# Performance work log

Measured on AMD Instinct MI355X. Metric: run time of the kernel, lower is better.

The kernel has to match this reference:

```python
import jax, jax.numpy as jnp
import numpy as np
import math

B, T, D_MODEL, N_HEADS = 4, 2048, 1024, 16
D_HEAD = D_MODEL // N_HEADS


def _rope_freqs(t, d_head):
    inv = 1.0 / (10000.0 ** (np.arange(0, d_head, 2, dtype=np.float32) / d_head))
    ang = np.arange(t, dtype=np.float32)[:, None] * inv[None, :]  # (T, d_head//2)
    return jnp.asarray(np.cos(ang)), jnp.asarray(np.sin(ang))


def setup_inputs() -> dict:
    key = jax.random.key(0)
    k1, k2, k3, k4, k5 = jax.random.split(key, 5)
    s = 1.0 / math.sqrt(D_MODEL)
    x = jax.random.normal(k1, (B, T, D_MODEL), dtype=jnp.float32)
    mask = jnp.triu(jnp.ones((T, T), dtype=bool), k=1)  # causal: mask future positions
    freqs_cos, freqs_sin = _rope_freqs(T, D_HEAD)
    qkv_w = jax.random.uniform(k2, (3 * D_MODEL, D_MODEL), jnp.float32, -s, s)
    qkv_b = jax.random.uniform(k3, (3 * D_MODEL,), jnp.float32, -s, s)
    proj_w = jax.random.uniform(k4, (D_MODEL, D_MODEL), jnp.float32, -s, s)
    proj_b = jax.random.uniform(k5, (D_MODEL,), jnp.float32, -s, s)
    return {"x": x, "mask": mask, "freqs_cos": freqs_cos, "freqs_sin": freqs_sin,
            "qkv_w": qkv_w, "qkv_b": qkv_b, "proj_w": proj_w, "proj_b": proj_b}


def _apply_rope(t, cos, sin):
    # t: (B, H, T, D_HEAD); cos/sin: (T, D_HEAD//2), broadcast over B, H
    tp = t.reshape(*t.shape[:-1], -1, 2)
    a, b = tp[..., 0], tp[..., 1]
    out_r = a * cos - b * sin
    out_i = a * sin + b * cos
    return jnp.stack([out_r, out_i], axis=-1).reshape(t.shape)


def reference(x, mask, freqs_cos, freqs_sin, qkv_w, qkv_b, proj_w, proj_b):
    Bx, Tx, C = x.shape
    qkv = x @ qkv_w.T + qkv_b  # (B, T, 3C)
    q, k, v = jnp.split(qkv, 3, axis=-1)
    def heads(z):
        return z.reshape(Bx, Tx, N_HEADS, D_HEAD).transpose(0, 2, 1, 3)  # (B,H,T,dh)
    q, k, v = heads(q), heads(k), heads(v)
    q = _apply_rope(q, freqs_cos, freqs_sin)
    k = _apply_rope(k, freqs_cos, freqs_sin)
    att = jnp.einsum('bhqd,bhkd->bhqk', q, k) / math.sqrt(D_HEAD)
    att = jnp.where(mask, -jnp.inf, att)
    att = jax.nn.softmax(att, axis=-1)
    out = jnp.einsum('bhqk,bhkd->bhqd', att, v)
    out = out.transpose(0, 2, 1, 3).reshape(Bx, Tx, C)
    return out @ proj_w.T + proj_b
```

## Files before the change

### kernel.cpp

```cpp
#include <hip/hip_runtime.h>
#include <stdint.h>

#define BB 4
#define TT 2048
#define CC 1024
#define HH 16
#define DH 64
#define NQKV 3072

typedef __bf16 bf16_t;
typedef __attribute__((ext_vector_type(8))) __bf16 bf16x8;
typedef __attribute__((ext_vector_type(4))) float f32x4;

#define MFMA16(a, b, c) __builtin_amdgcn_mfma_f32_16x16x32_bf16((a), (b), (c), 0, 0, 0)

__device__ __forceinline__ void gll16(const void* g, void* l) {
  typedef const __attribute__((address_space(1))) void* gp_t;
  typedef __attribute__((address_space(3))) void* lp_t;
  __builtin_amdgcn_global_load_lds((gp_t)(uintptr_t)g, (lp_t)(uintptr_t)l, 16, 0, 0);
}

__global__ __launch_bounds__(256) void cvt_k(const float* __restrict__ src,
                                             bf16_t* __restrict__ dst, int n) {
  const int i8 = (blockIdx.x * 256 + threadIdx.x) * 8;
  if (i8 < n) {
    const f32x4 a = *(const f32x4*)(src + i8);
    const f32x4 b = *(const f32x4*)(src + i8 + 4);
    bf16x8 r;
    r[0] = (bf16_t)a[0]; r[1] = (bf16_t)a[1]; r[2] = (bf16_t)a[2]; r[3] = (bf16_t)a[3];
    r[4] = (bf16_t)b[0]; r[5] = (bf16_t)b[1]; r[6] = (bf16_t)b[2]; r[7] = (bf16_t)b[3];
    *(bf16x8*)(dst + i8) = r;
  }
}

template <int EPI>
__global__ __launch_bounds__(256) void gemm_k(
    const bf16_t* __restrict__ A, const bf16_t* __restrict__ W,
    const float* __restrict__ bias,
    const float* __restrict__ fcos, const float* __restrict__ fsin,
    void* __restrict__ out0v, bf16_t* __restrict__ out1,
    bf16_t* __restrict__ out2) {
  __shared__ bf16_t Alds[2][128 * 32];
  __shared__ bf16_t Blds[2][128 * 32];
  const int K = 1024;
  const int tid = threadIdx.x;
  const int lane = tid & 63, wave = tid >> 6;
  const int quad = lane >> 4, c = lane & 15;
  const int wm = wave >> 1, wn = wave & 1;
  const int mbase = blockIdx.y * 128, nbase = blockIdx.x * 128;

  f32x4 acc[4][4];
#pragma unroll
  for (int i = 0; i < 4; ++i)
#pragma unroll
    for (int j = 0; j < 4; ++j) acc[i][j] = (f32x4){0.f, 0.f, 0.f, 0.f};

  const int ch0 = tid, ch1 = tid + 256;
  const bf16_t* ag0 = A + (mbase + (ch0 >> 2)) * K + (ch0 & 3) * 8;
  const bf16_t* ag1 = A + (mbase + (ch1 >> 2)) * K + (ch1 & 3) * 8;
  const bf16_t* bg0 = W + (nbase + (ch0 >> 2)) * K + (ch0 & 3) * 8;
  const bf16_t* bg1 = W + (nbase + (ch1 >> 2)) * K + (ch1 & 3) * 8;

  for (int k0 = 0; k0 < K; k0 += 64) {
    __syncthreads();
    gll16(ag0 + k0, &Alds[0][ch0 * 8]);
    gll16(ag1 + k0, &Alds[0][ch1 * 8]);
    gll16(bg0 + k0, &Blds[0][ch0 * 8]);
    gll16(bg1 + k0, &Blds[0][ch1 * 8]);
    gll16(ag0 + k0 + 32, &Alds[1][ch0 * 8]);
    gll16(ag1 + k0 + 32, &Alds[1][ch1 * 8]);
    gll16(bg0 + k0 + 32, &Blds[1][ch0 * 8]);
    gll16(bg1 + k0 + 32, &Blds[1][ch1 * 8]);
    __syncthreads();
#pragma unroll
    for (int half = 0; half < 2; ++half) {
      bf16x8 af[4], bfr[4];
#pragma unroll
      for (int mi = 0; mi < 4; ++mi)
        af[mi] = *(const bf16x8*)&Alds[half][(wm * 64 + mi * 16 + c) * 32 + quad * 8];
#pragma unroll
      for (int ni = 0; ni < 4; ++ni)
        bfr[ni] = *(const bf16x8*)&Blds[half][(wn * 64 + ni * 16 + c) * 32 + quad * 8];
#pragma unroll
      for (int mi = 0; mi < 4; ++mi)
#pragma unroll
        for (int ni = 0; ni < 4; ++ni)
          acc[mi][ni] = MFMA16(af[mi], bfr[ni], acc[mi][ni]);
    }
  }

  const float qscale = 0.18033688011112042f;
#pragma unroll
  for (int mi = 0; mi < 4; ++mi) {
#pragma unroll
    for (int ni = 0; ni < 4; ++ni) {
      const int n = nbase + wn * 64 + ni * 16 + c;
      const float bv = bias[n];
#pragma unroll
      for (int r = 0; r < 4; ++r) {
        const int m = mbase + wm * 64 + mi * 16 + quad * 4 + r;
        float v = acc[mi][ni][r] + bv;
        if (EPI == 0) {
          bf16_t* out0 = (bf16_t*)out0v;
          const int sel = n >> 10;
          const int nl = n & 1023;
          const int h = nl >> 6, d = nl & 63;
          const int b = m >> 11, t = m & 2047;
          const int dst = ((b * HH + h) * TT + t) * DH + d;
          if (sel < 2) {
            const float pv = __shfl_xor(v, 1, 64);
            const int d2 = d >> 1;
            const float cs = fcos[t * 32 + d2];
            const float sn = fsin[t * 32 + d2];
            float o = ((d & 1) == 0) ? (v * cs - pv * sn) : (pv * sn + v * cs);
            if (sel == 0) {
              o *= qscale;
              out0[dst] = (bf16_t)o;
            } else {
              out1[dst] = (bf16_t)o;
            }
          } else {
            out2[dst] = (bf16_t)v;
          }
        } else {
          float* outf = (float*)out0v;
          outf[m * CC + n] = v;
        }
      }
    }
  }
}

__global__ __launch_bounds__(256, 4) void attn_k(const bf16_t* __restrict__ Q,
                                                 const bf16_t* __restrict__ Kv,
                                                 const bf16_t* __restrict__ V,
                                                 bf16_t* __restrict__ O) {
  __shared__ bf16_t KS[2][64 * 64];
  __shared__ bf16_t VtS[2][64 * 64];
  __shared__ bf16_t PS[4][16 * 64];

  const int tid = threadIdx.x;
  const int lane = tid & 63, wave = tid >> 6;
  const int quad = lane >> 4, c = lane & 15;
  const int bi = blockIdx.x;
  const int pair = bi & 15, h = (bi >> 4) & 15, b = bi >> 8;
  const int qtA = pair, qtB = 31 - pair;
  const int nA = qtA + 1;

  const bf16_t* Qh = Q + ((b * HH + h) * TT) * DH;
  const bf16_t* Kh = Kv + ((b * HH + h) * TT) * DH;
  const bf16_t* Vh = V + ((b * HH + h) * TT) * DH;

  const f32x4 zero4 = {0.f, 0.f, 0.f, 0.f};
  bf16x8 ones8;
#pragma unroll
  for (int i = 0; i < 8; ++i) ones8[i] = (bf16_t)1.0f;

  const int krow0 = tid >> 3, kc8 = tid & 7, krow1 = krow0 + 32;
  const bf16_t* kbase0 = Kh + krow0 * DH + kc8 * 8;
  const bf16_t* kbase1 = Kh + krow1 * DH + kc8 * 8;
  const int vsb = tid >> 2, vjp = tid & 3;
  const int vrg = vsb & 7, vc8 = vsb >> 3;
  const int vd0 = vc8 * 8 + vjp * 2, vd1 = vd0 + 1;
  const bf16_t* vbase = Vh + vrg * 8 * DH + vd0;

  const int sw = c & 7;
  const int e0 = c * 64 + (quad ^ sw) * 8;
  const int e1 = c * 64 + ((quad + 4) ^ sw) * 8;

  bf16x8 kr0, kr1;
  uint32_t vr[8];
  auto load_tile = [&](int eoff) {
    kr0 = *(const bf16x8*)(kbase0 + eoff);
    kr1 = *(const bf16x8*)(kbase1 + eoff);
    const bf16_t* vp = vbase + eoff;
#pragma unroll
    for (int i = 0; i < 8; ++i) vr[i] = *(const uint32_t*)(vp + i * DH);
  };
  auto store_tile = [&](int buf) {
    *(bf16x8*)&KS[buf][(krow0 * 8 + (kc8 ^ (krow0 & 7))) * 8] = kr0;
    *(bf16x8*)&KS[buf][(krow1 * 8 + (kc8 ^ (krow1 & 7))) * 8] = kr1;
    union { bf16x8 v; uint16_t u[8]; } colA, colB;
#pragma unroll
    for (int i = 0; i < 8; ++i) {
      colA.u[i] = (uint16_t)(vr[i] & 0xffffu);
      colB.u[i] = (uint16_t)(vr[i] >> 16);
    }
    *(bf16x8*)&VtS[buf][(vd0 * 8 + (vrg ^ (vd0 & 7))) * 8] = colA.v;
    *(bf16x8*)&VtS[buf][(vd1 * 8 + (vrg ^ (vd1 & 7))) * 8] = colB.v;
  };

  int qtbase = qtA * 64;
  bf16x8 qf0 = *(const bf16x8*)(Qh + (qtbase + wave * 16 + c) * DH + quad * 8);
  bf16x8 qf1 = *(const bf16x8*)(Qh + (qtbase + wave * 16 + c) * DH + 32 + quad * 8);

  f32x4 o_acc[4] = {zero4, zero4, zero4, zero4};
  float m_r[4] = {-1e30f, -1e30f, -1e30f, -1e30f};
  float l_r[4] = {0.f, 0.f, 0.f, 0.f};

  auto write_O = [&](int qtb) {
#pragma unroll
    for (int r = 0; r < 4; ++r) {
      const int qg = qtb + wave * 16 + quad * 4 + r;
      const float inv = 1.0f / l_r[r];
#pragma unroll
      for (int ni = 0; ni < 4; ++ni)
        O[(b * TT + qg) * CC + h * 64 + ni * 16 + c] =
            (bf16_t)(o_acc[ni][r] * inv);
    }
  };

  load_tile(0);
  store_tile(0);
  __syncthreads();
  int coff = 0;
  int kkey = 0;

#define ATTN_ITER(FI, CUR)                                                     \
  {                                                                            \
    const int fi_ = (FI);                                                      \
    const bool pre_ = fi_ < 32;                                                \
    const int noff_ = (fi_ + 1 == nA) ? 0 : coff + 64 * DH;                    \
    if (pre_) load_tile(noff_);                                                \
    bf16x8 kf0[4], kf1[4];                                                     \
    _Pragma("unroll") for (int ni = 0; ni < 4; ++ni) {                         \
      kf0[ni] = *(const bf16x8*)&KS[CUR][ni * 1024 + e0];                      \
      kf1[ni] = *(const bf16x8*)&KS[CUR][ni * 1024 + e1];                      \
    }                                                                          \
    f32x4 s[4];                                                                \
    _Pragma("unroll") for (int ni = 0; ni < 4; ++ni) {                         \
      f32x4 t = MFMA16(qf0, kf0[ni], zero4);                                   \
      t = MFMA16(qf1, kf1[ni], t);                                             \
      s[ni] = t;                                                               \
    }                                                                          \
    const int minq_ = qtbase + wave * 16;                                      \
    if (kkey + 63 > minq_) {                                                   \
      _Pragma("unroll") for (int ni = 0; ni < 4; ++ni)                         \
          _Pragma("unroll") for (int r = 0; r < 4; ++r) {                      \
        const int key_ = kkey + ni * 16 + c;                                   \
        const int qg_ = minq_ + quad * 4 + r;                                  \
        if (key_ > qg_) s[ni][r] = -1e30f;                                     \
      }                                                                        \
    }                                                                          \
    float alpha[4];                                                            \
    _Pragma("unroll") for (int r = 0; r < 4; ++r) {                            \
      float mx = fmaxf(fmaxf(s[0][r], s[1][r]), fmaxf(s[2][r], s[3][r]));      \
      mx = fmaxf(mx, __shfl_xor(mx, 1, 64));                                   \
      mx = fmaxf(mx, __shfl_xor(mx, 2, 64));                                   \
      mx = fmaxf(mx, __shfl_xor(mx, 4, 64));                                   \
      mx = fmaxf(mx, __shfl_xor(mx, 8, 64));                                   \
      const float mnew = fmaxf(m_r[r], mx);                                    \
      alpha[r] = __builtin_amdgcn_exp2f(m_r[r] - mnew);                        \
      m_r[r] = mnew;                                                           \
    }                                                                          \
    _Pragma("unroll") for (int ni = 0; ni < 4; ++ni)                           \
        _Pragma("unroll") for (int r = 0; r < 4; ++r) {                        \
      const float p = __builtin_amdgcn_exp2f(s[ni][r] - m_r[r]);               \
      const int prow_ = quad * 4 + r, pcol_ = ni * 16 + c;                     \
      PS[wave][(prow_ * 8 + ((pcol_ >> 3) ^ (prow_ & 7))) * 8 + (pcol_ & 7)] = \
          (bf16_t)p;                                                           \
    }                                                                          \
    _Pragma("unroll") for (int r = 0; r < 4; ++r) {                            \
      _Pragma("unroll") for (int ni = 0; ni < 4; ++ni)                         \
          o_acc[ni][r] *= alpha[r];                                            \
    }                                                                          \
    asm volatile("s_waitcnt lgkmcnt(0)" ::: "memory");                         \
    const bf16x8 p0 = *(const bf16x8*)&PS[wave][e0];                           \
    const bf16x8 p1 = *(const bf16x8*)&PS[wave][e1];                           \
    f32x4 rs = MFMA16(p0, ones8, zero4);                                       \
    rs = MFMA16(p1, ones8, rs);                                                \
    _Pragma("unroll") for (int ni = 0; ni < 4; ++ni) {                         \
      const bf16x8 v0 = *(const bf16x8*)&VtS[CUR][ni * 1024 + e0];             \
      const bf16x8 v1 = *(const bf16x8*)&VtS[CUR][ni * 1024 + e1];             \
      o_acc[ni] = MFMA16(p0, v0, o_acc[ni]);                                   \
      o_acc[ni] = MFMA16(p1, v1, o_acc[ni]);                                   \
    }                                                                          \
    _Pragma("unroll") for (int r = 0; r < 4; ++r)                              \
        l_r[r] = l_r[r] * alpha[r] + rs[r];                                    \
    if (fi_ == nA - 1) {                                                       \
      write_O(qtbase);                                                         \
      qtbase = qtB * 64;                                                       \
      qf0 = *(const bf16x8*)(Qh + (qtbase + wave * 16 + c) * DH + quad * 8);   \
      qf1 = *(const bf16x8*)(Qh + (qtbase + wave * 16 + c) * DH + 32 +         \
                             quad * 8);                                        \
      _Pragma("unroll") for (int r = 0; r < 4; ++r) {                          \
        m_r[r] = -1e30f;                                                       \
        l_r[r] = 0.f;                                                          \
      }                                                                        \
      _Pragma("unroll") for (int ni = 0; ni < 4; ++ni) o_acc[ni] = zero4;      \
    }                                                                          \
    if (pre_) store_tile(1 - (CUR));                                           \
    __syncthreads();                                                           \
    coff = noff_;                                                              \
    kkey = (fi_ + 1 == nA) ? 0 : kkey + 64;                                    \
  }

  for (int fj = 0; fj < 16; ++fj) {
    ATTN_ITER(2 * fj, 0)
    ATTN_ITER(2 * fj + 1, 1)
  }
  ATTN_ITER(32, 0)
#undef ATTN_ITER

  write_O(qtbase);
}

extern "C" void kernel_launch(void* const* d_in, const int* in_sizes, int n_in,
                              void* d_out, int out_size, void* d_ws,
                              size_t ws_size, hipStream_t stream) {
  const float *x = nullptr, *fcos = nullptr, *fsin = nullptr;
  const float *qkv_w = nullptr, *qkv_b = nullptr, *proj_w = nullptr, *proj_b = nullptr;
  for (int i = 0; i < n_in; ++i) {
    const int s = in_sizes[i];
    const float* p = (const float*)d_in[i];
    if (s == BB * TT * CC) x = p;
    else if (s == TT * (DH / 2)) { if (!fcos) fcos = p; else fsin = p; }
    else if (s == NQKV * CC) qkv_w = p;
    else if (s == NQKV) qkv_b = p;
    else if (s == CC * CC) proj_w = p;
    else if (s == CC) proj_b = p;
  }

  const size_t NE = (size_t)BB * TT * CC;
  bf16_t* Qb = (bf16_t*)d_ws;
  bf16_t* Kb = Qb + NE;
  bf16_t* Vb = Kb + NE;
  bf16_t* Ob = Vb + NE;
  bf16_t* xb = Ob;
  bf16_t* wqkvb = (bf16_t*)d_out;
  bf16_t* wpb = Qb;

  cvt_k<<<dim3((int)(NE / 2048)), 256, 0, stream>>>(x, xb, (int)NE);
  cvt_k<<<dim3(NQKV * CC / 2048), 256, 0, stream>>>(qkv_w, wqkvb, NQKV * CC);

  gemm_k<0><<<dim3(NQKV / 128, (BB * TT) / 128), 256, 0, stream>>>(
      xb, wqkvb, qkv_b, fcos, fsin, (void*)Qb, Kb, Vb);
  attn_k<<<dim3(BB * HH * 16), 256, 0, stream>>>(Qb, Kb, Vb, Ob);
  cvt_k<<<dim3(CC * CC / 2048), 256, 0, stream>>>(proj_w, wpb, CC * CC);
  gemm_k<1><<<dim3(CC / 128, (BB * TT) / 128), 256, 0, stream>>>(
      Ob, wpb, proj_b, nullptr, nullptr, d_out, nullptr, nullptr);
}
```

Before: 329.5 us.

## Swizzle GEMM LDS tiles and read attention K fragments directly from global

Measured after the change: 397.7 us. 1.21x slower.

```diff
diff --git a/kernel.cpp b/kernel.cpp
--- a/kernel.cpp
+++ b/kernel.cpp
@@ -55,32 +55,38 @@
 #pragma unroll
     for (int j = 0; j < 4; ++j) acc[i][j] = (f32x4){0.f, 0.f, 0.f, 0.f};
 
-  const int ch0 = tid, ch1 = tid + 256;
-  const bf16_t* ag0 = A + (mbase + (ch0 >> 2)) * K + (ch0 & 3) * 8;
-  const bf16_t* ag1 = A + (mbase + (ch1 >> 2)) * K + (ch1 & 3) * 8;
-  const bf16_t* bg0 = W + (nbase + (ch0 >> 2)) * K + (ch0 & 3) * 8;
-  const bf16_t* bg1 = W + (nbase + (ch1 >> 2)) * K + (ch1 & 3) * 8;
+  const int s0 = tid, s1 = tid + 256;
+  const int r0 = s0 >> 2, cc0 = (s0 & 3) ^ (r0 & 3);
+  const int r1 = s1 >> 2, cc1 = (s1 & 3) ^ (r1 & 3);
+  const bf16_t* ag0 = A + (mbase + r0) * K + cc0 * 8;
+  const bf16_t* ag1 = A + (mbase + r1) * K + cc1 * 8;
+  const bf16_t* bg0 = W + (nbase + r0) * K + cc0 * 8;
+  const bf16_t* bg1 = W + (nbase + r1) * K + cc1 * 8;
 
   for (int k0 = 0; k0 < K; k0 += 64) {
     __syncthreads();
-    gll16(ag0 + k0, &Alds[0][ch0 * 8]);
-    gll16(ag1 + k0, &Alds[0][ch1 * 8]);
-    gll16(bg0 + k0, &Blds[0][ch0 * 8]);
-    gll16(bg1 + k0, &Blds[0][ch1 * 8]);
-    gll16(ag0 + k0 + 32, &Alds[1][ch0 * 8]);
-    gll16(ag1 + k0 + 32, &Alds[1][ch1 * 8]);
-    gll16(bg0 + k0 + 32, &Blds[1][ch0 * 8]);
-    gll16(bg1 + k0 + 32, &Blds[1][ch1 * 8]);
+    gll16(ag0 + k0, &Alds[0][s0 * 8]);
+    gll16(ag1 + k0, &Alds[0][s1 * 8]);
+    gll16(bg0 + k0, &Blds[0][s0 * 8]);
+    gll16(bg1 + k0, &Blds[0][s1 * 8]);
+    gll16(ag0 + k0 + 32, &Alds[1][s0 * 8]);
+    gll16(ag1 + k0 + 32, &Alds[1][s1 * 8]);
+    gll16(bg0 + k0 + 32, &Blds[1][s0 * 8]);
+    gll16(bg1 + k0 + 32, &Blds[1][s1 * 8]);
     __syncthreads();
 #pragma unroll
     for (int half = 0; half < 2; ++half) {
       bf16x8 af[4], bfr[4];
 #pragma unroll
-      for (int mi = 0; mi < 4; ++mi)
-        af[mi] = *(const bf16x8*)&Alds[half][(wm * 64 + mi * 16 + c) * 32 + quad * 8];
-#pragma unroll
-      for (int ni = 0; ni < 4; ++ni)
-        bfr[ni] = *(const bf16x8*)&Blds[half][(wn * 64 + ni * 16 + c) * 32 + quad * 8];
+      for (int mi = 0; mi < 4; ++mi) {
+        const int row = wm * 64 + mi * 16 + c;
+        af[mi] = *(const bf16x8*)&Alds[half][(row * 4 + (quad ^ (row & 3))) * 8];
+      }
+#pragma unroll
+      for (int ni = 0; ni < 4; ++ni) {
+        const int row = wn * 64 + ni * 16 + c;
+        bfr[ni] = *(const bf16x8*)&Blds[half][(row * 4 + (quad ^ (row & 3))) * 8];
+      }
 #pragma unroll
       for (int mi = 0; mi < 4; ++mi)
 #pragma unroll
@@ -135,7 +141,6 @@
                                                  const bf16_t* __restrict__ Kv,
                                                  const bf16_t* __restrict__ V,
                                                  bf16_t* __restrict__ O) {
-  __shared__ bf16_t KS[2][64 * 64];
   __shared__ bf16_t VtS[2][64 * 64];
   __shared__ bf16_t PS[4][16 * 64];
 
@@ -156,9 +161,6 @@
 #pragma unroll
   for (int i = 0; i < 8; ++i) ones8[i] = (bf16_t)1.0f;
 
-  const int krow0 = tid >> 3, kc8 = tid & 7, krow1 = krow0 + 32;
-  const bf16_t* kbase0 = Kh + krow0 * DH + kc8 * 8;
-  const bf16_t* kbase1 = Kh + krow1 * DH + kc8 * 8;
   const int vsb = tid >> 2, vjp = tid & 3;
   const int vrg = vsb & 7, vc8 = vsb >> 3;
   const int vd0 = vc8 * 8 + vjp * 2, vd1 = vd0 + 1;
@@ -167,19 +169,15 @@
   const int sw = c & 7;
   const int e0 = c * 64 + (quad ^ sw) * 8;
   const int e1 = c * 64 + ((quad + 4) ^ sw) * 8;
-
-  bf16x8 kr0, kr1;
+  const int koff = c * DH + quad * 8;
+
   uint32_t vr[8];
   auto load_tile = [&](int eoff) {
-    kr0 = *(const bf16x8*)(kbase0 + eoff);
-    kr1 = *(const bf16x8*)(kbase1 + eoff);
     const bf16_t* vp = vbase + eoff;
 #pragma unroll
     for (int i = 0; i < 8; ++i) vr[i] = *(const uint32_t*)(vp + i * DH);
   };
   auto store_tile = [&](int buf) {
-    *(bf16x8*)&KS[buf][(krow0 * 8 + (kc8 ^ (krow0 & 7))) * 8] = kr0;
-    *(bf16x8*)&KS[buf][(krow1 * 8 + (kc8 ^ (krow1 & 7))) * 8] = kr1;
     union { bf16x8 v; uint16_t u[8]; } colA, colB;
 #pragma unroll
     for (int i = 0; i < 8; ++i) {
@@ -222,10 +220,11 @@
     const bool pre_ = fi_ < 32;                                                \
     const int noff_ = (fi_ + 1 == nA) ? 0 : coff + 64 * DH;                    \
     if (pre_) load_tile(noff_);                                                \
+    const bf16_t* kt_ = Kh + kkey * DH + koff;                                 \
     bf16x8 kf0[4], kf1[4];                                                     \
     _Pragma("unroll") for (int ni = 0; ni < 4; ++ni) {                         \
-      kf0[ni] = *(const bf16x8*)&KS[CUR][ni * 1024 + e0];                      \
-      kf1[ni] = *(const bf16x8*)&KS[CUR][ni * 1024 + e1];                      \
+      kf0[ni] = *(const bf16x8*)(kt_ + ni * 16 * DH);                          \
+      kf1[ni] = *(const bf16x8*)(kt_ + ni * 16 * DH + 32);                     \
     }                                                                          \
     f32x4 s[4];                                                                \
     _Pragma("unroll") for (int ni = 0; ni < 4; ++ni) {                         \
```
